# Optimization experiments

Hardware: AMD Instinct MI355X
Metric: run time of the kernel (lower is better)

Reference implementation:

```python
import jax, jax.numpy as jnp
import numpy as np

N, D, H, M = 8192, 64, 4096, 2
EPS = 1e-12  # F.normalize eps


def setup_inputs() -> dict:
    key = jax.random.key(0)
    k0, k1, k2, k3, k4 = jax.random.split(key, 5)
    # spins in {-1, +1}
    x = (2 * jax.random.randint(k0, (N, D), 0, 2) - 1).astype(jnp.float32)
    W1 = jax.random.normal(k1, (D, H), jnp.float32) * 0.05
    b1 = jax.random.normal(k2, (H,), jnp.float32) * 0.05
    W2 = jax.random.normal(k3, (H, M), jnp.float32) * 0.05
    b2 = jax.random.normal(k4, (M,), jnp.float32) * 0.05
    return {"x": x, "W1": W1, "b1": b1, "W2": W2, "b2": b2}


def reference(x, W1, b1, W2, b2):
    # Per step d: mask off sites >= d, run MLP, L2-normalize the 2 amplitudes,
    # select psi_pos/psi_neg by the spin at site d, accumulate product.
    n, d_sites = x.shape
    site_idx = jnp.arange(d_sites)

    def step(wav, d):
        mask = (site_idx < d).astype(x.dtype)          # [D], sites 0..d-1 visible
        h = jnp.tanh((x * mask) @ W1 + b1)             # [N, H]
        out = jnp.tanh(h @ W2 + b2)                    # [N, 2]
        norm = jnp.maximum(
            jnp.sqrt(jnp.sum(out * out, axis=1, keepdims=True)), EPS)
        out = out / norm                               # F.normalize(out, 2)
        sel = jnp.where(x[:, d] > 0, out[:, 0], out[:, 1])
        return wav * sel, None

    wav0 = jnp.ones((n,), x.dtype)
    wav, _ = jax.lax.scan(step, wav0, jnp.arange(d_sites))
    return wav
```

## Files before the change

kernel.cpp:

```cpp
#include <hip/hip_runtime.h>
#include <math.h>

#define NS 8192
#define DS 64
#define HD 4096
#define C2L 2.8853900817779268f

typedef float v2f __attribute__((ext_vector_type(2)));

__device__ __forceinline__ v2f pk_add(v2f a, v2f b) {
    v2f d; asm("v_pk_add_f32 %0, %1, %2" : "=v"(d) : "v"(a), "v"(b)); return d;
}
__device__ __forceinline__ v2f pk_mul(v2f a, v2f b) {
    v2f d; asm("v_pk_mul_f32 %0, %1, %2" : "=v"(d) : "v"(a), "v"(b)); return d;
}
__device__ __forceinline__ v2f pk_fma(v2f a, v2f b, v2f c) {
    v2f d; asm("v_pk_fma_f32 %0, %1, %2, %3" : "=v"(d) : "v"(a), "v"(b), "v"(c)); return d;
}

__device__ __forceinline__ float fast_tanh(float x) {
    float t = __builtin_amdgcn_exp2f(x * C2L);
    float r = __builtin_amdgcn_rcpf(t + 1.0f);
    return __builtin_fmaf(-2.0f, r, 1.0f);
}

__device__ __forceinline__ float swz_xor16(float v) {
    return __int_as_float(__builtin_amdgcn_ds_swizzle(__float_as_int(v), 0x401F));
}
__device__ __forceinline__ float swz_xor8(float v) {
    return __int_as_float(__builtin_amdgcn_ds_swizzle(__float_as_int(v), 0x201F));
}
__device__ __forceinline__ float bperm(int addr, float v) {
    return __int_as_float(__builtin_amdgcn_ds_bpermute(addr, __float_as_int(v)));
}

__global__ __launch_bounds__(256) void qnade_prep_E(
    const float* __restrict__ W1, float* __restrict__ Ep, float* __restrict__ Em)
{
    int i = blockIdx.x * 256 + threadIdx.x;
    float w = W1[i] * C2L;
    Ep[i] = __builtin_amdgcn_exp2f(w);
    Em[i] = __builtin_amdgcn_exp2f(-w);
}

__global__ __launch_bounds__(256) void qnade_prep_S(
    const float* __restrict__ W2, const float* __restrict__ b2, float* __restrict__ C01)
{
    __shared__ float p0[4], p1[4];
    int tid = threadIdx.x;
    float s0 = 0.0f, s1 = 0.0f;
    for (int h = tid; h < HD; h += 256) {
        float2 w = ((const float2*)W2)[h];
        s0 += w.x; s1 += w.y;
    }
    #pragma unroll
    for (int m = 1; m < 64; m <<= 1) {
        s0 += __shfl_xor(s0, m, 64);
        s1 += __shfl_xor(s1, m, 64);
    }
    if ((tid & 63) == 0) { p0[tid >> 6] = s0; p1[tid >> 6] = s1; }
    __syncthreads();
    if (tid == 0) {
        C01[0] = p0[0] + p0[1] + p0[2] + p0[3] + b2[0];
        C01[1] = p1[0] + p1[1] + p1[2] + p1[3] + b2[1];
    }
}

__global__ __launch_bounds__(256) void qnade_main(
    const float* __restrict__ x, const float* __restrict__ b1,
    const float* __restrict__ W2, const float* __restrict__ Ep,
    const float* __restrict__ Em, const float* __restrict__ C01,
    float* __restrict__ out)
{
    __shared__ float parts[DS * 64];

    const int tid  = threadIdx.x;
    const int lane = tid & 63;
    const int wv   = tid >> 6;
    const int n    = blockIdx.x;
    const int hbase = wv * 1024 + lane * 4;
    const int bp_addr = ((lane ^ 32) << 2);

    v2f w20[8], w21[8];
    #pragma unroll
    for (int q = 0; q < 4; ++q) {
        const float4* p = (const float4*)(W2 + 2 * (hbase + q * 256));
        float4 A = p[0], B = p[1];
        w20[2*q]   = (v2f){A.x, A.z};  w21[2*q]   = (v2f){A.y, A.w};
        w20[2*q+1] = (v2f){B.x, B.z};  w21[2*q+1] = (v2f){B.y, B.w};
    }

    v2f t2[8];
    #pragma unroll
    for (int q = 0; q < 4; ++q) {
        float4 b = *(const float4*)(b1 + hbase + q * 256);
        t2[2*q]   = (v2f){__builtin_amdgcn_exp2f(b.x * C2L), __builtin_amdgcn_exp2f(b.y * C2L)};
        t2[2*q+1] = (v2f){__builtin_amdgcn_exp2f(b.z * C2L), __builtin_amdgcn_exp2f(b.w * C2L)};
    }

    const float xv = x[n * DS + lane];
    const unsigned long long msk = __ballot(xv > 0.0f);
    const float* EpL = Ep + hbase;
    const float* EmL = Em + hbase;

    #pragma unroll 2
    for (int d = 0; d < DS; ++d) {
        const float* E = (((msk >> d) & 1ull) ? EpL : EmL) + d * HD;
        float4 e0 = *(const float4*)(E);
        float4 e1 = *(const float4*)(E + 256);
        float4 e2 = *(const float4*)(E + 512);
        float4 e3 = *(const float4*)(E + 768);

        v2f p2[8];
        p2[0] = pk_add(t2[0], (v2f){1.0f, 1.0f});
        #pragma unroll
        for (int j = 1; j < 8; ++j) p2[j] = pk_fma(p2[j - 1], t2[j], p2[j - 1]);

        float P = p2[7].x * p2[7].y;
        float R = __builtin_amdgcn_rcpf(P);
        v2f RR = (v2f){R * p2[7].y, R * p2[7].x};

        v2f acc0, acc1;
        {
            v2f r = pk_mul(RR, p2[6]);
            acc0 = pk_mul(r, w20[7]);
            acc1 = pk_mul(r, w21[7]);
            RR = pk_fma(RR, t2[7], RR);
        }
        #pragma unroll
        for (int j = 6; j >= 1; --j) {
            v2f r = pk_mul(RR, p2[j - 1]);
            acc0 = pk_fma(r, w20[j], acc0);
            acc1 = pk_fma(r, w21[j], acc1);
            RR = pk_fma(RR, t2[j], RR);
        }
        acc0 = pk_fma(RR, w20[0], acc0);
        acc1 = pk_fma(RR, w21[0], acc1);

        t2[0] = pk_mul(t2[0], (v2f){e0.x, e0.y});
        t2[1] = pk_mul(t2[1], (v2f){e0.z, e0.w});
        t2[2] = pk_mul(t2[2], (v2f){e1.x, e1.y});
        t2[3] = pk_mul(t2[3], (v2f){e1.z, e1.w});
        t2[4] = pk_mul(t2[4], (v2f){e2.x, e2.y});
        t2[5] = pk_mul(t2[5], (v2f){e2.z, e2.w});
        t2[6] = pk_mul(t2[6], (v2f){e3.x, e3.y});
        t2[7] = pk_mul(t2[7], (v2f){e3.z, e3.w});

        float a0 = acc0.x + acc0.y;
        float a1 = acc1.x + acc1.y;
        a0 += bperm(bp_addr, a0);
        a1 += bperm(bp_addr, a1);
        a0 += swz_xor16(a0);
        a1 += swz_xor16(a1);
        a0 += swz_xor8(a0);
        a1 += swz_xor8(a1);
        if (lane < 8)
            *(float2*)&parts[d * 64 + wv * 16 + lane * 2] = make_float2(a0, a1);
    }

    __syncthreads();

    if (tid < DS) {
        const int d = tid;
        const float* p = parts + d * 64;
        float s0 = 0.0f, s1 = 0.0f;
        #pragma unroll
        for (int w = 0; w < 4; ++w) {
            #pragma unroll
            for (int i = 0; i < 8; ++i) {
                s0 += p[w * 16 + 2 * i];
                s1 += p[w * 16 + 2 * i + 1];
            }
        }
        float dot0 = __builtin_fmaf(-2.0f, s0, C01[0]);
        float dot1 = __builtin_fmaf(-2.0f, s1, C01[1]);
        float o0 = fast_tanh(dot0);
        float o1 = fast_tanh(dot1);
        float nrm = sqrtf(__builtin_fmaf(o0, o0, o1 * o1));
        nrm = fmaxf(nrm, 1e-12f);
        float sel = (x[n * DS + d] > 0.0f) ? o0 : o1;
        float v = sel * __builtin_amdgcn_rcpf(nrm);
        v *= __shfl_xor(v, 1, 64);
        v *= __shfl_xor(v, 2, 64);
        v *= __shfl_xor(v, 4, 64);
        v *= __shfl_xor(v, 8, 64);
        v *= __shfl_xor(v, 16, 64);
        v *= __shfl_xor(v, 32, 64);
        if (tid == 0) out[n] = v;
    }
}

__global__ __launch_bounds__(256) void qnade_fallback(
    const float* __restrict__ x, const float* __restrict__ W1,
    const float* __restrict__ b1, const float* __restrict__ W2,
    const float* __restrict__ b2, float* __restrict__ out)
{
    __shared__ __align__(16) float w20s[HD];
    __shared__ __align__(16) float w21s[HD];
    const int tid = threadIdx.x;
    for (int i = tid; i < HD; i += 256) {
        float2 w = ((const float2*)W2)[i];
        w20s[i] = w.x;
        w21s[i] = w.y;
    }
    const int lane = tid & 63;
    const int wv   = tid >> 6;
    const int n    = (blockIdx.x << 2) + wv;
    const float b20 = b2[0];
    const float b21 = b2[1];
    const float xv = x[n * DS + lane];
    float4 a[16];
    const float4* b1v = (const float4*)b1;
    #pragma unroll
    for (int q = 0; q < 16; ++q) a[q] = b1v[q * 64 + lane];
    __syncthreads();
    const float4* w20v = (const float4*)w20s;
    const float4* w21v = (const float4*)w21s;
    float wav = 1.0f;
    for (int d = 0; d < DS; ++d) {
        const float xd = __shfl(xv, d, 64);
        const float4* w1v = (const float4*)(W1 + d * HD);
        float dot0 = 0.0f, dot1 = 0.0f;
        #pragma unroll
        for (int q = 0; q < 16; ++q) {
            float4 w1 = w1v[q * 64 + lane];
            float4 av = a[q];
            float h0 = fast_tanh(av.x);
            float h1 = fast_tanh(av.y);
            float h2 = fast_tanh(av.z);
            float h3 = fast_tanh(av.w);
            float4 c0 = w20v[q * 64 + lane];
            float4 c1 = w21v[q * 64 + lane];
            dot0 = fmaf(h0, c0.x, dot0); dot0 = fmaf(h1, c0.y, dot0);
            dot0 = fmaf(h2, c0.z, dot0); dot0 = fmaf(h3, c0.w, dot0);
            dot1 = fmaf(h0, c1.x, dot1); dot1 = fmaf(h1, c1.y, dot1);
            dot1 = fmaf(h2, c1.z, dot1); dot1 = fmaf(h3, c1.w, dot1);
            av.x = fmaf(xd, w1.x, av.x); av.y = fmaf(xd, w1.y, av.y);
            av.z = fmaf(xd, w1.z, av.z); av.w = fmaf(xd, w1.w, av.w);
            a[q] = av;
        }
        #pragma unroll
        for (int m = 1; m < 64; m <<= 1) {
            dot0 += __shfl_xor(dot0, m, 64);
            dot1 += __shfl_xor(dot1, m, 64);
        }
        float o0 = fast_tanh(dot0 + b20);
        float o1 = fast_tanh(dot1 + b21);
        float nrm = sqrtf(fmaf(o0, o0, o1 * o1));
        nrm = fmaxf(nrm, 1e-12f);
        float sel = (xd > 0.0f) ? o0 : o1;
        wav *= sel / nrm;
    }
    out[n] = wav;
}

extern "C" void kernel_launch(void* const* d_in, const int* in_sizes, int n_in,
                              void* d_out, int out_size, void* d_ws, size_t ws_size,
                              hipStream_t stream) {
    const float* x  = (const float*)d_in[0];
    const float* W1 = (const float*)d_in[1];
    const float* b1 = (const float*)d_in[2];
    const float* W2 = (const float*)d_in[3];
    const float* b2 = (const float*)d_in[4];
    float* out = (float*)d_out;

    const size_t need = (size_t)(2 * DS * HD + 2) * sizeof(float);
    if (ws_size >= need) {
        float* Ep  = (float*)d_ws;
        float* Em  = Ep + DS * HD;
        float* C01 = Em + DS * HD;
        hipLaunchKernelGGL(qnade_prep_E, dim3(DS * HD / 256), dim3(256), 0, stream, W1, Ep, Em);
        hipLaunchKernelGGL(qnade_prep_S, dim3(1), dim3(256), 0, stream, W2, b2, C01);
        hipLaunchKernelGGL(qnade_main, dim3(NS), dim3(256), 0, stream, x, b1, W2, Ep, Em, C01, out);
    } else {
        hipLaunchKernelGGL(qnade_fallback, dim3(NS / 4), dim3(256), 0, stream, x, W1, b1, W2, b2, out);
    }
}
```

Measured before the change: 458.3 us.

## Batch per-step cross-lane reductions into chunked shared-memory transposed reduction

Instead of doing a bpermute plus two swizzle reductions per site step inside the serial loop, each thread writes its per-step partial sums to shared memory. Every 8 steps the whole block reduces the 8 rows cooperatively, with 32 threads per row and swizzle trees. The Ep/Em tables are merged into one buffer indexed by an unsigned offset, which removes the pointer select. The aim is to take cross-lane traffic off the per-step critical path, at the cost of two block barriers per chunk.

Result: faster. 423.9 us (-7.5%).

```diff
diff --git a/kernel.cpp b/kernel.cpp
--- a/kernel.cpp
+++ b/kernel.cpp
@@ -5,6 +5,8 @@
 #define DS 64
 #define HD 4096
 #define C2L 2.8853900817779268f
+#define CH 8
+#define NCH (DS / CH)
 
 typedef float v2f __attribute__((ext_vector_type(2)));
 
@@ -24,23 +26,21 @@
     return __builtin_fmaf(-2.0f, r, 1.0f);
 }
 
-__device__ __forceinline__ float swz_xor16(float v) {
-    return __int_as_float(__builtin_amdgcn_ds_swizzle(__float_as_int(v), 0x401F));
-}
-__device__ __forceinline__ float swz_xor8(float v) {
-    return __int_as_float(__builtin_amdgcn_ds_swizzle(__float_as_int(v), 0x201F));
-}
-__device__ __forceinline__ float bperm(int addr, float v) {
-    return __int_as_float(__builtin_amdgcn_ds_bpermute(addr, __float_as_int(v)));
+template <int PATT>
+__device__ __forceinline__ v2f swz_xor(v2f v) {
+    v2f d;
+    d.x = __int_as_float(__builtin_amdgcn_ds_swizzle(__float_as_int(v.x), PATT));
+    d.y = __int_as_float(__builtin_amdgcn_ds_swizzle(__float_as_int(v.y), PATT));
+    return d;
 }
 
 __global__ __launch_bounds__(256) void qnade_prep_E(
-    const float* __restrict__ W1, float* __restrict__ Ep, float* __restrict__ Em)
+    const float* __restrict__ W1, float* __restrict__ Et)
 {
     int i = blockIdx.x * 256 + threadIdx.x;
     float w = W1[i] * C2L;
-    Ep[i] = __builtin_amdgcn_exp2f(w);
-    Em[i] = __builtin_amdgcn_exp2f(-w);
+    Et[i]           = __builtin_amdgcn_exp2f(w);
+    Et[DS * HD + i] = __builtin_amdgcn_exp2f(-w);
 }
 
 __global__ __launch_bounds__(256) void qnade_prep_S(
@@ -68,18 +68,17 @@
 
 __global__ __launch_bounds__(256) void qnade_main(
     const float* __restrict__ x, const float* __restrict__ b1,
-    const float* __restrict__ W2, const float* __restrict__ Ep,
-    const float* __restrict__ Em, const float* __restrict__ C01,
-    float* __restrict__ out)
-{
-    __shared__ float parts[DS * 64];
+    const float* __restrict__ W2, const float* __restrict__ Et,
+    const float* __restrict__ C01, float* __restrict__ out)
+{
+    __shared__ float2 parts[CH][256];
+    __shared__ float2 fin[DS];
 
     const int tid  = threadIdx.x;
     const int lane = tid & 63;
     const int wv   = tid >> 6;
     const int n    = blockIdx.x;
     const int hbase = wv * 1024 + lane * 4;
-    const int bp_addr = ((lane ^ 32) << 2);
 
     v2f w20[8], w21[8];
     #pragma unroll
@@ -100,85 +99,86 @@
 
     const float xv = x[n * DS + lane];
     const unsigned long long msk = __ballot(xv > 0.0f);
-    const float* EpL = Ep + hbase;
-    const float* EmL = Em + hbase;
-
-    #pragma unroll 2
-    for (int d = 0; d < DS; ++d) {
-        const float* E = (((msk >> d) & 1ull) ? EpL : EmL) + d * HD;
-        float4 e0 = *(const float4*)(E);
-        float4 e1 = *(const float4*)(E + 256);
-        float4 e2 = *(const float4*)(E + 512);
-        float4 e3 = *(const float4*)(E + 768);
-
-        v2f p2[8];
-        p2[0] = pk_add(t2[0], (v2f){1.0f, 1.0f});
-        #pragma unroll
-        for (int j = 1; j < 8; ++j) p2[j] = pk_fma(p2[j - 1], t2[j], p2[j - 1]);
-
-        float P = p2[7].x * p2[7].y;
-        float R = __builtin_amdgcn_rcpf(P);
-        v2f RR = (v2f){R * p2[7].y, R * p2[7].x};
-
-        v2f acc0, acc1;
+
+    int d = 0;
+    for (int c = 0; c < NCH; ++c) {
+        #pragma unroll 2
+        for (int s8 = 0; s8 < CH; ++s8, ++d) {
+            const unsigned uoff = (((msk >> d) & 1ull) ? 0u : (unsigned)(DS * HD)) + d * HD;
+            const float* E = Et + uoff + hbase;
+            float4 e0 = *(const float4*)(E);
+            float4 e1 = *(const float4*)(E + 256);
+            float4 e2 = *(const float4*)(E + 512);
+            float4 e3 = *(const float4*)(E + 768);
+
+            v2f p2[8];
+            p2[0] = pk_add(t2[0], (v2f){1.0f, 1.0f});
+            #pragma unroll
+            for (int j = 1; j < 8; ++j) p2[j] = pk_fma(p2[j - 1], t2[j], p2[j - 1]);
+
+            float P = p2[7].x * p2[7].y;
+            float R = __builtin_amdgcn_rcpf(P);
+            v2f RR = (v2f){R * p2[7].y, R * p2[7].x};
+
+            v2f acc0, acc1;
+            {
+                v2f r = pk_mul(RR, p2[6]);
+                acc0 = pk_mul(r, w20[7]);
+                acc1 = pk_mul(r, w21[7]);
+                RR = pk_fma(RR, t2[7], RR);
+            }
+            #pragma unroll
+            for (int j = 6; j >= 1; --j) {
+                v2f r = pk_mul(RR, p2[j - 1]);
+                acc0 = pk_fma(r, w20[j], acc0);
+                acc1 = pk_fma(r, w21[j], acc1);
+                RR = pk_fma(RR, t2[j], RR);
+            }
+            acc0 = pk_fma(RR, w20[0], acc0);
+            acc1 = pk_fma(RR, w21[0], acc1);
+
+            t2[0] = pk_mul(t2[0], (v2f){e0.x, e0.y});
+            t2[1] = pk_mul(t2[1], (v2f){e0.z, e0.w});
+            t2[2] = pk_mul(t2[2], (v2f){e1.x, e1.y});
+            t2[3] = pk_mul(t2[3], (v2f){e1.z, e1.w});
+            t2[4] = pk_mul(t2[4], (v2f){e2.x, e2.y});
+            t2[5] = pk_mul(t2[5], (v2f){e2.z, e2.w});
+            t2[6] = pk_mul(t2[6], (v2f){e3.x, e3.y});
+            t2[7] = pk_mul(t2[7], (v2f){e3.z, e3.w});
+
+            parts[s8][tid] = make_float2(acc0.x + acc0.y, acc1.x + acc1.y);
+        }
+
+        __syncthreads();
         {
-            v2f r = pk_mul(RR, p2[6]);
-            acc0 = pk_mul(r, w20[7]);
-            acc1 = pk_mul(r, w21[7]);
-            RR = pk_fma(RR, t2[7], RR);
-        }
-        #pragma unroll
-        for (int j = 6; j >= 1; --j) {
-            v2f r = pk_mul(RR, p2[j - 1]);
-            acc0 = pk_fma(r, w20[j], acc0);
-            acc1 = pk_fma(r, w21[j], acc1);
-            RR = pk_fma(RR, t2[j], RR);
-        }
-        acc0 = pk_fma(RR, w20[0], acc0);
-        acc1 = pk_fma(RR, w21[0], acc1);
-
-        t2[0] = pk_mul(t2[0], (v2f){e0.x, e0.y});
-        t2[1] = pk_mul(t2[1], (v2f){e0.z, e0.w});
-        t2[2] = pk_mul(t2[2], (v2f){e1.x, e1.y});
-        t2[3] = pk_mul(t2[3], (v2f){e1.z, e1.w});
-        t2[4] = pk_mul(t2[4], (v2f){e2.x, e2.y});
-        t2[5] = pk_mul(t2[5], (v2f){e2.z, e2.w});
-        t2[6] = pk_mul(t2[6], (v2f){e3.x, e3.y});
-        t2[7] = pk_mul(t2[7], (v2f){e3.z, e3.w});
-
-        float a0 = acc0.x + acc0.y;
-        float a1 = acc1.x + acc1.y;
-        a0 += bperm(bp_addr, a0);
-        a1 += bperm(bp_addr, a1);
-        a0 += swz_xor16(a0);
-        a1 += swz_xor16(a1);
-        a0 += swz_xor8(a0);
-        a1 += swz_xor8(a1);
-        if (lane < 8)
-            *(float2*)&parts[d * 64 + wv * 16 + lane * 2] = make_float2(a0, a1);
-    }
-
-    __syncthreads();
+            const int sr = tid >> 5;
+            const int k  = tid & 31;
+            v2f s = (v2f){0.0f, 0.0f};
+            #pragma unroll
+            for (int j = 0; j < 8; ++j) {
+                float2 v = parts[sr][k + 32 * j];
+                s = pk_add(s, (v2f){v.x, v.y});
+            }
+            s = pk_add(s, swz_xor<0x041F>(s));
+            s = pk_add(s, swz_xor<0x081F>(s));
+            s = pk_add(s, swz_xor<0x101F>(s));
+            s = pk_add(s, swz_xor<0x201F>(s));
+            s = pk_add(s, swz_xor<0x401F>(s));
+            if (k == 0) fin[c * CH + sr] = make_float2(s.x, s.y);
+        }
+        __syncthreads();
+    }
 
     if (tid < DS) {
-        const int d = tid;
-        const float* p = parts + d * 64;
-        float s0 = 0.0f, s1 = 0.0f;
-        #pragma unroll
-        for (int w = 0; w < 4; ++w) {
-            #pragma unroll
-            for (int i = 0; i < 8; ++i) {
-                s0 += p[w * 16 + 2 * i];
-                s1 += p[w * 16 + 2 * i + 1];
-            }
-        }
-        float dot0 = __builtin_fmaf(-2.0f, s0, C01[0]);
-        float dot1 = __builtin_fmaf(-2.0f, s1, C01[1]);
+        const int dd = tid;
+        float2 sv = fin[dd];
+        float dot0 = __builtin_fmaf(-2.0f, sv.x, C01[0]);
+        float dot1 = __builtin_fmaf(-2.0f, sv.y, C01[1]);
         float o0 = fast_tanh(dot0);
         float o1 = fast_tanh(dot1);
         float nrm = sqrtf(__builtin_fmaf(o0, o0, o1 * o1));
         nrm = fmaxf(nrm, 1e-12f);
-        float sel = (x[n * DS + d] > 0.0f) ? o0 : o1;
+        float sel = (x[n * DS + dd] > 0.0f) ? o0 : o1;
         float v = sel * __builtin_amdgcn_rcpf(nrm);
         v *= __shfl_xor(v, 1, 64);
         v *= __shfl_xor(v, 2, 64);
@@ -266,12 +266,11 @@
 
     const size_t need = (size_t)(2 * DS * HD + 2) * sizeof(float);
     if (ws_size >= need) {
-        float* Ep  = (float*)d_ws;
-        float* Em  = Ep + DS * HD;
-        float* C01 = Em + DS * HD;
-        hipLaunchKernelGGL(qnade_prep_E, dim3(DS * HD / 256), dim3(256), 0, stream, W1, Ep, Em);
+        float* Et  = (float*)d_ws;
+        float* C01 = Et + 2 * DS * HD;
+        hipLaunchKernelGGL(qnade_prep_E, dim3(DS * HD / 256), dim3(256), 0, stream, W1, Et);
         hipLaunchKernelGGL(qnade_prep_S, dim3(1), dim3(256), 0, stream, W2, b2, C01);
-        hipLaunchKernelGGL(qnade_main, dim3(NS), dim3(256), 0, stream, x, b1, W2, Ep, Em, C01, out);
+        hipLaunchKernelGGL(qnade_main, dim3(NS), dim3(256), 0, stream, x, b1, W2, Et, C01, out);
     } else {
         hipLaunchKernelGGL(qnade_fallback, dim3(NS / 4), dim3(256), 0, stream, x, W1, b1, W2, b2, out);
     }
```
